# Kernel tuning notes

Hardware: AMD Instinct MI355X
Metric: run time of the kernel (lower is better)

## Reference

```python
import jax, jax.numpy as jnp
import numpy as np

X_DIM = 362
N_EXPERTS = 3
HIDDEN = [1024, 2048, 2048, 1024]  # layer widths; final layer maps back to X_DIM


def _init_params(key):
    dims = [X_DIM] + HIDDEN + [X_DIM]
    params = {}
    for li in range(len(dims) - 1):
        fan_in = dims[li]
        kW, kb, key = jax.random.split(key, 3)
        bound = 1.0 / np.sqrt(fan_in)
        # stacked over experts: [E, in, out]
        params[f"W{li}"] = jax.random.uniform(kW, (N_EXPERTS, dims[li], dims[li + 1]), jnp.float32, -bound, bound)
        params[f"b{li}"] = jax.random.uniform(kb, (N_EXPERTS, dims[li + 1]), jnp.float32, -bound, bound)
    return params


def setup_inputs() -> dict:
    key = jax.random.key(0)
    kx, kn, ka, kp = jax.random.split(key, 4)
    B = 8192
    inp = {
        "batch_x": jax.random.normal(kx, (B, X_DIM), jnp.float32),
        "batch_next": jax.random.normal(kn, (B, X_DIM), jnp.float32),
        "batch_a": jax.random.randint(ka, (B,), 0, N_EXPERTS, jnp.int64),
    }
    inp.update(_init_params(kp))
    return inp


def _experts_forward(x, W0, b0, W1, b1, W2, b2, W3, b3, W4, b4):
    # Run every expert on the full batch (dense grouped GEMMs), then select.
    # h: [E, B, d]
    h = jax.nn.relu(jnp.einsum("bi,eio->ebo", x, W0) + b0[:, None, :])
    h = jax.nn.relu(jnp.einsum("ebi,eio->ebo", h, W1) + b1[:, None, :])
    h = jax.nn.relu(jnp.einsum("ebi,eio->ebo", h, W2) + b2[:, None, :])
    h = jax.nn.relu(jnp.einsum("ebi,eio->ebo", h, W3) + b3[:, None, :])
    return jnp.einsum("ebi,eio->ebo", h, W4) + b4[:, None, :]  # [E, B, X_DIM]


def reference(batch_x, batch_next, batch_a, W0, b0, W1, b1, W2, b2, W3, b3, W4, b4):
    preds = _experts_forward(batch_x, W0, b0, W1, b1, W2, b2, W3, b3, W4, b4)
    # route: pick each sample's prediction from its action's expert
    pred_next = preds[batch_a, jnp.arange(batch_x.shape[0])]  # [B, X_DIM]
    return jnp.mean((pred_next - batch_next) ** 2)
```

## Files before the change

### kernel.cpp

```cpp
#include <hip/hip_runtime.h>
#include <hip/hip_bf16.h>

#define B_SZ   8192
#define XD     362
#define NEXP   3
#define NTILES 70
#define MP     (NTILES*128)

typedef __bf16 bf16x8 __attribute__((ext_vector_type(8)));
typedef float  f32x4  __attribute__((ext_vector_type(4)));

__device__ __forceinline__ unsigned short f2bf(float f) {
    unsigned u = __float_as_uint(f);
    u += 0x7fffu + ((u >> 16) & 1u);
    return (unsigned short)(u >> 16);
}

__global__ __launch_bounds__(1024) void k_route(const int* __restrict__ a,
                                                int* __restrict__ hdr,
                                                int* __restrict__ row_of) {
    __shared__ int sc[3][1024];
    int tid = threadIdx.x;
    int ev[8];
    int c0 = 0, c1 = 0, c2 = 0;
#pragma unroll
    for (int j = 0; j < 8; ++j) {
        int e = a[tid * 8 + j];
        ev[j] = e;
        c0 += (e == 0); c1 += (e == 1); c2 += (e == 2);
    }
    sc[0][tid] = c0; sc[1][tid] = c1; sc[2][tid] = c2;
    __syncthreads();
    for (int off = 1; off < 1024; off <<= 1) {
        int v0 = (tid >= off) ? sc[0][tid - off] : 0;
        int v1 = (tid >= off) ? sc[1][tid - off] : 0;
        int v2 = (tid >= off) ? sc[2][tid - off] : 0;
        __syncthreads();
        sc[0][tid] += v0; sc[1][tid] += v1; sc[2][tid] += v2;
        __syncthreads();
    }
    int tot0 = sc[0][1023], tot1 = sc[1][1023], tot2 = sc[2][1023];
    int t0 = ((tot0 + 255) >> 8) << 1;
    int t1 = ((tot1 + 255) >> 8) << 1;
    int t2 = ((tot2 + 255) >> 8) << 1;
    int seg0 = 0, seg1 = t0 * 128, seg2 = (t0 + t1) * 128;
    int nt = t0 + t1 + t2;
    int b0 = seg0 + sc[0][tid] - c0;
    int b1 = seg1 + sc[1][tid] - c1;
    int b2 = seg2 + sc[2][tid] - c2;
#pragma unroll
    for (int j = 0; j < 8; ++j) {
        int e = ev[j];
        int pos = (e == 0) ? b0++ : (e == 1) ? b1++ : b2++;
        row_of[pos] = tid * 8 + j;
    }
    if (tid == 0) {
        hdr[0] = tot0; hdr[1] = tot1; hdr[2] = tot2;
        hdr[6] = seg0; hdr[7] = seg1; hdr[8] = seg2;
        hdr[12] = nt;
        hdr[13] = nt / 2 - 1;
        hdr[16] = 0;
    }
    if (tid < NTILES)
        hdr[32 + tid] = (tid < t0) ? 0 : (tid < t0 + t1) ? 1 : (tid < nt) ? 2 : -1;
    for (int r = tid; r < MP; r += 1024) {
        int pad;
        if (r < seg1)           pad = (r - seg0) >= tot0;
        else if (r < seg2)      pad = (r - seg1) >= tot1;
        else if (r < nt * 128)  pad = (r - seg2) >= tot2;
        else                    pad = 1;
        if (pad) row_of[r] = -1;
    }
}

__global__ void k_gather(const float* __restrict__ x, const int* __restrict__ row_of,
                         unsigned short* __restrict__ xg) {
    int r = blockIdx.x;
    int c = threadIdx.x;
    int orig = row_of[r];
    float v = (orig >= 0 && c < XD) ? x[(size_t)orig * XD + c] : 0.f;
    xg[(size_t)r * 384 + c] = f2bf(v);
}

__global__ void k_transpose(const float* __restrict__ W, unsigned short* __restrict__ Wt,
                            int K, int N, int Kp, int Np) {
    __shared__ float t[64][33];
    int e  = blockIdx.z;
    int kb = blockIdx.x * 64, nb = blockIdx.y * 32;
    const float* We = W + (size_t)e * K * N;
    unsigned short* Wte = Wt + (size_t)e * Np * Kp;
    int tx = threadIdx.x, ty = threadIdx.y;
#pragma unroll
    for (int j = 0; j < 8; ++j) {
        int k = kb + ty + j * 8, n = nb + tx;
        t[ty + j * 8][tx] = (k < K && n < N) ? We[(size_t)k * N + n] : 0.f;
    }
    __syncthreads();
#pragma unroll
    for (int j = 0; j < 4; ++j) {
        int n = ty + j * 8;
        unsigned int lo = f2bf(t[2 * tx][n]);
        unsigned int hi = f2bf(t[2 * tx + 1][n]);
        *(unsigned int*)&Wte[(size_t)(nb + n) * Kp + kb + 2 * tx] = lo | (hi << 16);
    }
}

template <int TM, int TN, int WAVES, bool FINAL, bool TAIL, bool SKIPLAST>
__global__ __launch_bounds__(WAVES * 64) void k_gemm(
    const unsigned short* __restrict__ A, int lda,
    const unsigned short* __restrict__ Bt, int K, int Np,
    const float* __restrict__ bias, int nvalid,
    unsigned short* __restrict__ C, int ldc,
    const int* __restrict__ hdr,
    const float* __restrict__ nextv, const int* __restrict__ row_of,
    float* __restrict__ accum)
{
    __shared__ unsigned short As[2][TM * 64];
    __shared__ unsigned short Bs[2][TN * 64];
    __shared__ float red[WAVES];

    constexpr int WGN = TN / 64;
    constexpr int LA  = TM / (WAVES * 8);
    constexpr int LB  = TN / (WAVES * 8);

    int mt128;
    if constexpr (TAIL) {
        mt128 = hdr[13] * 2 + blockIdx.y;
    } else {
        if (SKIPLAST && (int)blockIdx.y >= hdr[13] && TM == 256) return;
        mt128 = blockIdx.y * (TM / 128);
    }
    int e = hdr[32 + mt128];
    if (e < 0) return;
    int row0 = mt128 * 128;
    int n0   = blockIdx.x * TN;

    int tid  = threadIdx.x;
    int wid  = tid >> 6, lane = tid & 63;
    int quad = lane >> 4, l15 = lane & 15;
    int sw   = l15 & 7;
    int wm = (wid / WGN) * 64, wn = (wid % WGN) * 64;

    const unsigned short* Ag = A  + (size_t)row0 * lda;
    const unsigned short* Bg = Bt + (size_t)e * Np * K + (size_t)n0 * K;
    const float* be = bias + (size_t)e * nvalid;

    int srow = lane >> 3;
    int scol = ((lane & 7) ^ srow) * 8;

    f32x4 acc[4][4];
#pragma unroll
    for (int i = 0; i < 4; ++i)
#pragma unroll
        for (int j = 0; j < 4; ++j)
            acc[i][j] = (f32x4){0.f, 0.f, 0.f, 0.f};

#define STAGE(K0, P)                                                              \
    {                                                                             \
        _Pragma("unroll")                                                         \
        for (int ii = 0; ii < LA; ++ii) {                                         \
            int rbase = wid * (TM / WAVES) + ii * 8;                              \
            const unsigned short* gp = Ag + (size_t)(rbase + srow) * lda + (K0) + scol; \
            __builtin_amdgcn_global_load_lds(                                     \
                (const __attribute__((address_space(1))) void*)gp,                \
                (__attribute__((address_space(3))) void*)(As[P] + rbase * 64), 16, 0, 0); \
        }                                                                         \
        _Pragma("unroll")                                                         \
        for (int ii = 0; ii < LB; ++ii) {                                         \
            int rbase = wid * (TN / WAVES) + ii * 8;                              \
            const unsigned short* gp = Bg + (size_t)(rbase + srow) * K + (K0) + scol;   \
            __builtin_amdgcn_global_load_lds(                                     \
                (const __attribute__((address_space(1))) void*)gp,                \
                (__attribute__((address_space(3))) void*)(Bs[P] + rbase * 64), 16, 0, 0); \
        }                                                                         \
    }

#define COMPUTE(P)                                                                \
    {                                                                             \
        _Pragma("unroll")                                                         \
        for (int kh = 0; kh < 2; ++kh) {                                          \
            bf16x8 af[4], bfr[4];                                                 \
            _Pragma("unroll")                                                     \
            for (int f = 0; f < 4; ++f) {                                         \
                int row = wm + f * 16 + l15;                                      \
                af[f] = *(const bf16x8*)(As[P] + row * 64 + (((kh * 4 + quad) ^ sw) << 3)); \
            }                                                                     \
            _Pragma("unroll")                                                     \
            for (int f = 0; f < 4; ++f) {                                         \
                int row = wn + f * 16 + l15;                                      \
                bfr[f] = *(const bf16x8*)(Bs[P] + row * 64 + (((kh * 4 + quad) ^ sw) << 3)); \
            }                                                                     \
            _Pragma("unroll")                                                     \
            for (int fm = 0; fm < 4; ++fm)                                        \
                _Pragma("unroll")                                                 \
                for (int fn = 0; fn < 4; ++fn)                                    \
                    acc[fm][fn] = __builtin_amdgcn_mfma_f32_16x16x32_bf16(        \
                        af[fm], bfr[fn], acc[fm][fn], 0, 0, 0);                   \
        }                                                                         \
    }

    STAGE(0, 0);
    __syncthreads();
    for (int k0 = 0; k0 < K; k0 += 128) {
        if (k0 + 64 < K) STAGE(k0 + 64, 1);
        COMPUTE(0);
        __syncthreads();
        if (k0 + 128 < K) STAGE(k0 + 128, 0);
        COMPUTE(1);
        __syncthreads();
    }
#undef STAGE
#undef COMPUTE

    if constexpr (!FINAL) {
#pragma unroll
        for (int fn = 0; fn < 4; ++fn) {
            int n = n0 + wn + fn * 16 + l15;
            float bv = be[n];
#pragma unroll
            for (int fm = 0; fm < 4; ++fm) {
#pragma unroll
                for (int i = 0; i < 4; ++i) {
                    int r = row0 + wm + fm * 16 + quad * 4 + i;
                    float v = acc[fm][fn][i] + bv;
                    v = v > 0.f ? v : 0.f;
                    C[(size_t)r * ldc + n] = f2bf(v);
                }
            }
        }
    } else {
        float local = 0.f;
#pragma unroll
        for (int fm = 0; fm < 4; ++fm) {
#pragma unroll
            for (int i = 0; i < 4; ++i) {
                int r = row0 + wm + fm * 16 + quad * 4 + i;
                int orig = row_of[r];
                if (orig >= 0) {
                    const float* nrow = nextv + (size_t)orig * XD;
#pragma unroll
                    for (int fn = 0; fn < 4; ++fn) {
                        int n = n0 + wn + fn * 16 + l15;
                        if (n < XD) {
                            float v = acc[fm][fn][i] + be[n];
                            float d = v - nrow[n];
                            local += d * d;
                        }
                    }
                }
            }
        }
        for (int off = 32; off > 0; off >>= 1)
            local += __shfl_down(local, off, 64);
        if (lane == 0) red[wid] = local;
        __syncthreads();
        if (tid == 0) {
            float s = 0.f;
#pragma unroll
            for (int w = 0; w < WAVES; ++w) s += red[w];
            atomicAdd(accum, s);
        }
    }
}

__global__ void k_final(const int* hdr, float* out) {
    if (blockIdx.x == 0 && threadIdx.x == 0) {
        float s = ((const float*)hdr)[16];
        out[0] = s / (float)(B_SZ * XD);
    }
}

extern "C" void kernel_launch(void* const* d_in, const int* in_sizes, int n_in,
                              void* d_out, int out_size, void* d_ws, size_t ws_size,
                              hipStream_t stream) {
    const float* x     = (const float*)d_in[0];
    const float* nextv = (const float*)d_in[1];
    const int*   a     = (const int*)d_in[2];
    const float* W0 = (const float*)d_in[3],  *b0 = (const float*)d_in[4];
    const float* W1 = (const float*)d_in[5],  *b1 = (const float*)d_in[6];
    const float* W2 = (const float*)d_in[7],  *b2 = (const float*)d_in[8];
    const float* W3 = (const float*)d_in[9],  *b3 = (const float*)d_in[10];
    const float* W4 = (const float*)d_in[11], *b4 = (const float*)d_in[12];

    int* hdr    = (int*)d_ws;
    int* row_of = hdr + 128;
    unsigned short* xg = (unsigned short*)(row_of + MP);
    unsigned short* hA = xg + (size_t)MP * 384;
    unsigned short* hB = hA + (size_t)MP * 2048;
    unsigned short* Wt = hB + (size_t)MP * 2048;
    float* accum = (float*)(hdr + 16);

    k_route <<<1, 1024, 0, stream>>>(a, hdr, row_of);
    k_gather<<<MP, 384, 0, stream>>>(x, row_of, xg);

    k_transpose<<<dim3(6, 32, 3), dim3(32, 8), 0, stream>>>(W0, Wt, XD, 1024, 384, 1024);
    k_gemm<128, 128, 4, false, false, false><<<dim3(8, NTILES), 256, 0, stream>>>(
        xg, 384, Wt, 384, 1024, b0, 1024, hA, 1024, hdr, nullptr, nullptr, nullptr);

    k_transpose<<<dim3(16, 64, 3), dim3(32, 8), 0, stream>>>(W1, Wt, 1024, 2048, 1024, 2048);
    k_gemm<256, 256, 16, false, false, true><<<dim3(8, NTILES / 2), 1024, 0, stream>>>(
        hA, 1024, Wt, 1024, 2048, b1, 2048, hB, 2048, hdr, nullptr, nullptr, nullptr);
    k_gemm<128, 128, 4, false, true, false><<<dim3(16, 2), 256, 0, stream>>>(
        hA, 1024, Wt, 1024, 2048, b1, 2048, hB, 2048, hdr, nullptr, nullptr, nullptr);

    k_transpose<<<dim3(32, 64, 3), dim3(32, 8), 0, stream>>>(W2, Wt, 2048, 2048, 2048, 2048);
    k_gemm<256, 256, 16, false, false, true><<<dim3(8, NTILES / 2), 1024, 0, stream>>>(
        hB, 2048, Wt, 2048, 2048, b2, 2048, hA, 2048, hdr, nullptr, nullptr, nullptr);
    k_gemm<128, 128, 4, false, true, false><<<dim3(16, 2), 256, 0, stream>>>(
        hB, 2048, Wt, 2048, 2048, b2, 2048, hA, 2048, hdr, nullptr, nullptr, nullptr);

    k_transpose<<<dim3(32, 32, 3), dim3(32, 8), 0, stream>>>(W3, Wt, 2048, 1024, 2048, 1024);
    k_gemm<256, 256, 16, false, false, true><<<dim3(4, NTILES / 2), 1024, 0, stream>>>(
        hA, 2048, Wt, 2048, 1024, b3, 1024, hB, 1024, hdr, nullptr, nullptr, nullptr);
    k_gemm<128, 128, 4, false, true, false><<<dim3(8, 2), 256, 0, stream>>>(
        hA, 2048, Wt, 2048, 1024, b3, 1024, hB, 1024, hdr, nullptr, nullptr, nullptr);

    k_transpose<<<dim3(16, 12, 3), dim3(32, 8), 0, stream>>>(W4, Wt, 1024, XD, 1024, 384);
    k_gemm<128, 128, 4, true, false, false><<<dim3(3, NTILES), 256, 0, stream>>>(
        hB, 1024, Wt, 1024, 384, b4, XD, nullptr, 0, hdr, nextv, row_of, accum);

    k_final<<<1, 64, 0, stream>>>(hdr, (float*)d_out);
}
```

Baseline: 523.9 us.

## Merge weight transposes into one launch, use wave-shuffle scan, retile tail GEMMs

```diff
diff --git a/kernel.cpp b/kernel.cpp
--- a/kernel.cpp
+++ b/kernel.cpp
@@ -19,8 +19,9 @@
 __global__ __launch_bounds__(1024) void k_route(const int* __restrict__ a,
                                                 int* __restrict__ hdr,
                                                 int* __restrict__ row_of) {
-    __shared__ int sc[3][1024];
-    int tid = threadIdx.x;
+    __shared__ int wpre[3][16];
+    __shared__ int stot[3];
+    int tid = threadIdx.x, lane = tid & 63, w = tid >> 6;
     int ev[8];
     int c0 = 0, c1 = 0, c2 = 0;
 #pragma unroll
@@ -29,25 +30,36 @@
         ev[j] = e;
         c0 += (e == 0); c1 += (e == 1); c2 += (e == 2);
     }
-    sc[0][tid] = c0; sc[1][tid] = c1; sc[2][tid] = c2;
+    int i0 = c0, i1 = c1, i2 = c2;
+#pragma unroll
+    for (int off = 1; off < 64; off <<= 1) {
+        int t0_ = __shfl_up(i0, off, 64);
+        int t1_ = __shfl_up(i1, off, 64);
+        int t2_ = __shfl_up(i2, off, 64);
+        if (lane >= off) { i0 += t0_; i1 += t1_; i2 += t2_; }
+    }
+    if (lane == 63) { wpre[0][w] = i0; wpre[1][w] = i1; wpre[2][w] = i2; }
     __syncthreads();
-    for (int off = 1; off < 1024; off <<= 1) {
-        int v0 = (tid >= off) ? sc[0][tid - off] : 0;
-        int v1 = (tid >= off) ? sc[1][tid - off] : 0;
-        int v2 = (tid >= off) ? sc[2][tid - off] : 0;
-        __syncthreads();
-        sc[0][tid] += v0; sc[1][tid] += v1; sc[2][tid] += v2;
-        __syncthreads();
-    }
-    int tot0 = sc[0][1023], tot1 = sc[1][1023], tot2 = sc[2][1023];
+    if (tid == 0) {
+        int s0 = 0, s1 = 0, s2 = 0;
+#pragma unroll
+        for (int k = 0; k < 16; ++k) {
+            int a0 = wpre[0][k], a1 = wpre[1][k], a2 = wpre[2][k];
+            wpre[0][k] = s0; wpre[1][k] = s1; wpre[2][k] = s2;
+            s0 += a0; s1 += a1; s2 += a2;
+        }
+        stot[0] = s0; stot[1] = s1; stot[2] = s2;
+    }
+    __syncthreads();
+    int tot0 = stot[0], tot1 = stot[1], tot2 = stot[2];
     int t0 = ((tot0 + 255) >> 8) << 1;
     int t1 = ((tot1 + 255) >> 8) << 1;
     int t2 = ((tot2 + 255) >> 8) << 1;
     int seg0 = 0, seg1 = t0 * 128, seg2 = (t0 + t1) * 128;
     int nt = t0 + t1 + t2;
-    int b0 = seg0 + sc[0][tid] - c0;
-    int b1 = seg1 + sc[1][tid] - c1;
-    int b2 = seg2 + sc[2][tid] - c2;
+    int b0 = seg0 + wpre[0][w] + i0 - c0;
+    int b1 = seg1 + wpre[1][w] + i1 - c1;
+    int b2 = seg2 + wpre[2][w] + i2 - c2;
 #pragma unroll
     for (int j = 0; j < 8; ++j) {
         int e = ev[j];
@@ -82,27 +94,56 @@
     xg[(size_t)r * 384 + c] = f2bf(v);
 }
 
+__device__ __forceinline__ void transpose_tile(const float* __restrict__ We,
+                                               unsigned short* __restrict__ Wte,
+                                               int K, int N, int Kp,
+                                               int kb, int nb, int tx, int ty,
+                                               float (*t)[33]) {
+#pragma unroll
+    for (int j = 0; j < 8; ++j) {
+        int k = kb + ty + j * 8, n = nb + tx;
+        t[ty + j * 8][tx] = (k < K && n < N) ? We[(size_t)k * N + n] : 0.f;
+    }
+    __syncthreads();
+#pragma unroll
+    for (int j = 0; j < 4; ++j) {
+        int n = ty + j * 8;
+        unsigned int lo = f2bf(t[2 * tx][n]);
+        unsigned int hi = f2bf(t[2 * tx + 1][n]);
+        *(unsigned int*)&Wte[(size_t)(nb + n) * Kp + kb + 2 * tx] = lo | (hi << 16);
+    }
+}
+
 __global__ void k_transpose(const float* __restrict__ W, unsigned short* __restrict__ Wt,
                             int K, int N, int Kp, int Np) {
     __shared__ float t[64][33];
     int e  = blockIdx.z;
     int kb = blockIdx.x * 64, nb = blockIdx.y * 32;
-    const float* We = W + (size_t)e * K * N;
-    unsigned short* Wte = Wt + (size_t)e * Np * Kp;
-    int tx = threadIdx.x, ty = threadIdx.y;
-#pragma unroll
-    for (int j = 0; j < 8; ++j) {
-        int k = kb + ty + j * 8, n = nb + tx;
-        t[ty + j * 8][tx] = (k < K && n < N) ? We[(size_t)k * N + n] : 0.f;
-    }
-    __syncthreads();
-#pragma unroll
-    for (int j = 0; j < 4; ++j) {
-        int n = ty + j * 8;
-        unsigned int lo = f2bf(t[2 * tx][n]);
-        unsigned int hi = f2bf(t[2 * tx + 1][n]);
-        *(unsigned int*)&Wte[(size_t)(nb + n) * Kp + kb + 2 * tx] = lo | (hi << 16);
-    }
+    transpose_tile(W + (size_t)e * K * N, Wt + (size_t)e * Np * Kp,
+                   K, N, Kp, kb, nb, threadIdx.x, threadIdx.y, t);
+}
+
+#define WT_OFF0 0
+#define WT_OFF1 1179648u
+#define WT_OFF2 7471104u
+#define WT_OFF3 20054016u
+#define WT_OFF4 26345472u
+#define WT_TOTAL 27525120u
+
+__global__ void k_transpose_all(const float* __restrict__ W0, const float* __restrict__ W1,
+                                const float* __restrict__ W2, const float* __restrict__ W3,
+                                const float* __restrict__ W4, unsigned short* __restrict__ Wt) {
+    __shared__ float t[64][33];
+    int ti = blockIdx.x, e = blockIdx.z;
+    const float* W; int K, N, Kp, kt; unsigned off; int Np;
+    if (ti < 192)       { W = W0; K = 362;  N = 1024; Kp = 384;  Np = 1024; kt = 6;  off = WT_OFF0; }
+    else if (ti < 1216) { W = W1; K = 1024; N = 2048; Kp = 1024; Np = 2048; kt = 16; off = WT_OFF1; ti -= 192; }
+    else if (ti < 3264) { W = W2; K = 2048; N = 2048; Kp = 2048; Np = 2048; kt = 32; off = WT_OFF2; ti -= 1216; }
+    else if (ti < 4288) { W = W3; K = 2048; N = 1024; Kp = 2048; Np = 1024; kt = 32; off = WT_OFF3; ti -= 3264; }
+    else                { W = W4; K = 1024; N = 362;  Kp = 1024; Np = 384;  kt = 16; off = WT_OFF4; ti -= 4288; }
+    int kb = (ti % kt) * 64, nb = (ti / kt) * 32;
+    transpose_tile(W + (size_t)e * K * N, Wt + off + (size_t)e * Np * Kp,
+                   K, N, Kp, kb, nb, threadIdx.x, threadIdx.y, t);
 }
 
 template <int TM, int TN, int WAVES, bool FINAL, bool TAIL, bool SKIPLAST>
@@ -235,9 +276,9 @@
 #pragma unroll
             for (int i = 0; i < 4; ++i) {
                 int r = row0 + wm + fm * 16 + quad * 4 + i;
-                int orig = row_of[r];
-                if (orig >= 0) {
-                    const float* nrow = nextv + (size_t)orig * XD;
+                int orig_r = row_of[r];
+                if (orig_r >= 0) {
+                    const float* nrow = nextv + (size_t)orig_r * XD;
 #pragma unroll
                     for (int fn = 0; fn < 4; ++fn) {
                         int n = n0 + wn + fn * 16 + l15;
@@ -290,34 +331,44 @@
     unsigned short* Wt = hB + (size_t)MP * 2048;
     float* accum = (float*)(hdr + 16);
 
+    size_t base = (size_t)(128 + MP) * 4 + (size_t)MP * 384 * 2 + (size_t)MP * 2048 * 2 * 2;
+    bool merged = ws_size >= base + (size_t)WT_TOTAL * 2;
+
+    unsigned short *Wt0, *Wt1, *Wt2, *Wt3, *Wt4;
+    if (merged) {
+        Wt0 = Wt + WT_OFF0; Wt1 = Wt + WT_OFF1; Wt2 = Wt + WT_OFF2;
+        Wt3 = Wt + WT_OFF3; Wt4 = Wt + WT_OFF4;
+        k_transpose_all<<<dim3(4480, 1, 3), dim3(32, 8), 0, stream>>>(W0, W1, W2, W3, W4, Wt);
+    } else {
+        Wt0 = Wt1 = Wt2 = Wt3 = Wt4 = Wt;
+    }
+
     k_route <<<1, 1024, 0, stream>>>(a, hdr, row_of);
     k_gather<<<MP, 384, 0, stream>>>(x, row_of, xg);
 
-    k_transpose<<<dim3(6, 32, 3), dim3(32, 8), 0, stream>>>(W0, Wt, XD, 1024, 384, 1024);
+    if (!merged) k_transpose<<<dim3(6, 32, 3), dim3(32, 8), 0, stream>>>(W0, Wt0, XD, 1024, 384, 1024);
     k_gemm<128, 128, 4, false, false, false><<<dim3(8, NTILES), 256, 0, stream>>>(
-        xg, 384, Wt, 384, 1024, b0, 1024, hA, 1024, hdr, nullptr, nullptr, nullptr);
-
-    k_transpose<<<dim3(16, 64, 3), dim3(32, 8), 0, stream>>>(W1, Wt, 1024, 2048, 1024, 2048);
+        xg, 384, Wt0, 384, 1024, b0, 1024, hA, 1024, hdr, nullptr, nullptr, nullptr);
+
+    if (!merged) k_transpose<<<dim3(16, 64, 3), dim3(32, 8), 0, stream>>>(W1, Wt1, 1024, 2048, 1024, 2048);
     k_gemm<256, 256, 16, false, false, true><<<dim3(8, NTILES / 2), 1024, 0, stream>>>(
-        hA, 1024, Wt, 1024, 2048, b1, 2048, hB, 2048, hdr, nullptr, nullptr, nullptr);
-    k_gemm<128, 128, 4, false, true, false><<<dim3(16, 2), 256, 0, stream>>>(
-        hA, 1024, Wt, 1024, 2048, b1, 2048, hB, 2048, hdr, nullptr, nullptr, nullptr);
-
-    k_transpose<<<dim3(32, 64, 3), dim3(32, 8), 0, stream>>>(W2, Wt, 2048, 2048, 2048, 2048);
+        hA, 1024, Wt1, 1024, 2048, b1, 2048, hB, 2048, hdr, nullptr, nullptr, nullptr);
+    k_gemm<128, 256, 8, false, true, false><<<dim3(8, 2), 512, 0, stream>>>(
+        hA, 1024, Wt1, 1024, 2048, b1, 2048, hB, 2048, hdr, nullptr, nullptr, nullptr);
+
+    if (!merged) k_transpose<<<dim3(32, 64, 3), dim3(32, 8), 0, stream>>>(W2, Wt2, 2048, 2048, 2048, 2048);
     k_gemm<256, 256, 16, false, false, true><<<dim3(8, NTILES / 2), 1024, 0, stream>>>(
-        hB, 2048, Wt, 2048, 2048, b2, 2048, hA, 2048, hdr, nullptr, nullptr, nullptr);
-    k_gemm<128, 128, 4, false, true, false><<<dim3(16, 2), 256, 0, stream>>>(
-        hB, 2048, Wt, 2048, 2048, b2, 2048, hA, 2048, hdr, nullptr, nullptr, nullptr);
-
-    k_transpose<<<dim3(32, 32, 3), dim3(32, 8), 0, stream>>>(W3, Wt, 2048, 1024, 2048, 1024);
-    k_gemm<256, 256, 16, false, false, true><<<dim3(4, NTILES / 2), 1024, 0, stream>>>(
-        hA, 2048, Wt, 2048, 1024, b3, 1024, hB, 1024, hdr, nullptr, nullptr, nullptr);
-    k_gemm<128, 128, 4, false, true, false><<<dim3(8, 2), 256, 0, stream>>>(
-        hA, 2048, Wt, 2048, 1024, b3, 1024, hB, 1024, hdr, nullptr, nullptr, nullptr);
-
-    k_transpose<<<dim3(16, 12, 3), dim3(32, 8), 0, stream>>>(W4, Wt, 1024, XD, 1024, 384);
+        hB, 2048, Wt2, 2048, 2048, b2, 2048, hA, 2048, hdr, nullptr, nullptr, nullptr);
+    k_gemm<128, 256, 8, false, true, false><<<dim3(8, 2), 512, 0, stream>>>(
+        hB, 2048, Wt2, 2048, 2048, b2, 2048, hA, 2048, hdr, nullptr, nullptr, nullptr);
+
+    if (!merged) k_transpose<<<dim3(32, 32, 3), dim3(32, 8), 0, stream>>>(W3, Wt3, 2048, 1024, 2048, 1024);
+    k_gemm<128, 128, 4, false, false, false><<<dim3(8, NTILES), 256, 0, stream>>>(
+        hA, 2048, Wt3, 2048, 1024, b3, 1024, hB, 1024, hdr, nullptr, nullptr, nullptr);
+
+    if (!merged) k_transpose<<<dim3(16, 12, 3), dim3(32, 8), 0, stream>>>(W4, Wt4, 1024, XD, 1024, 384);
     k_gemm<128, 128, 4, true, false, false><<<dim3(3, NTILES), 256, 0, stream>>>(
-        hB, 1024, Wt, 1024, 384, b4, XD, nullptr, 0, hdr, nextv, row_of, accum);
+        hB, 1024, Wt4, 1024, 384, b4, XD, nullptr, 0, hdr, nextv, row_of, accum);
 
     k_final<<<1, 64, 0, stream>>>(hdr, (float*)d_out);
 }
```

Measured after the change: 505.3 us. -3.5%, faster.
